# Kernel tuning notes

Hardware: AMD Instinct MI355X
Metric: run time of the kernel (lower is better)

Reference implementation:

```python
import jax, jax.numpy as jnp
import numpy as np

NUM_CLASSES = 1000
MARGIN = 1.0
COS_EPS = 1e-8   # torch F.cosine_similarity eps
NORM_EPS = 1e-12 # torch F.normalize eps


def setup_inputs() -> dict:
    key = jax.random.key(0)
    k1, k2 = jax.random.split(key)
    N, D = 65536, 256
    embeddings = jax.random.normal(k1, (N, D), dtype=jnp.float32)
    labels = jax.random.randint(k2, (N,), 0, NUM_CLASSES)
    return {"embeddings": embeddings, "labels": labels}


def reference(embeddings, labels):
    N = embeddings.shape[0]
    # L2-normalize embeddings (torch F.normalize with eps clamp on norm)
    e_norm = jnp.maximum(jnp.linalg.norm(embeddings, axis=1, keepdims=True), NORM_EPS)
    e = embeddings / e_norm  # [N, D], unit rows

    # Per-class mean of normalized embeddings; zero vector for empty classes
    sums = jax.ops.segment_sum(e, labels, num_segments=NUM_CLASSES)          # [C, D]
    counts = jax.ops.segment_sum(jnp.ones((N,), e.dtype), labels,
                                 num_segments=NUM_CLASSES)                    # [C]
    centers = sums / jnp.maximum(counts, 1.0)[:, None]                        # [C, D]

    # cosine_similarity(e_i, center_j) = (e_i . c_j) / max(||e_i||*||c_j||, eps)
    # ||e_i|| == 1 (up to the normalize clamp), so denom = max(||c_j||, eps)
    c_norm = jnp.linalg.norm(centers, axis=1)                                 # [C]
    denom = jnp.maximum(c_norm, COS_EPS)
    sims = (e @ centers.T) / denom[None, :]                                   # [N, C]

    rows = jnp.arange(N)
    pos = jnp.square(sims[rows, labels] - 1.0)                                # [N]
    neg_all = jnp.square(jax.nn.relu(MARGIN - sims))                          # [N, C]
    neg_at_label = neg_all[rows, labels]                                      # [N]
    neg = (neg_all.sum(axis=1) - neg_at_label) / (NUM_CLASSES - 1)            # [N]

    return jnp.mean(pos + neg)
```

## Files before the change

kernel.cpp:

```cpp
#include <hip/hip_runtime.h>
#include <hip/hip_bf16.h>

#define NROWS 65536
#define DIM   256
#define NCLS  1000
#define CPAD  1024

typedef __attribute__((ext_vector_type(8))) short bf16x8;
typedef __attribute__((ext_vector_type(4))) float f32x4;

__device__ inline unsigned short f2bf(float x) {
    unsigned int u = __builtin_bit_cast(unsigned int, x);
    unsigned int lsb = (u >> 16) & 1u;
    u += 0x7fffu + lsb;
    return (unsigned short)(u >> 16);
}

__device__ inline float bf2f(unsigned short u) {
    unsigned int v = ((unsigned int)u) << 16;
    return __builtin_bit_cast(float, v);
}

__device__ inline void gload_lds16(const void* g, void* l) {
    __builtin_amdgcn_global_load_lds(
        (const __attribute__((address_space(1))) unsigned int*)g,
        (__attribute__((address_space(3))) unsigned int*)l, 16, 0, 0);
}

__global__ __launch_bounds__(256) void k_norm_acc(
    const float* __restrict__ emb, const int* __restrict__ labels,
    unsigned short* __restrict__ e, unsigned int* __restrict__ counts)
{
    int gid  = blockIdx.x * 256 + threadIdx.x;
    int row  = gid >> 6;
    int lane = gid & 63;
    float4 v = ((const float4*)(emb + (size_t)row * DIM))[lane];
    float ss = v.x*v.x + v.y*v.y + v.z*v.z + v.w*v.w;
    #pragma unroll
    for (int off = 1; off < 64; off <<= 1) ss += __shfl_xor(ss, off);
    float inv = 1.0f / fmaxf(sqrtf(ss), 1e-12f);
    v.x *= inv; v.y *= inv; v.z *= inv; v.w *= inv;
    ushort4 u;
    u.x = f2bf(v.x); u.y = f2bf(v.y); u.z = f2bf(v.z); u.w = f2bf(v.w);
    ((ushort4*)(e + (size_t)row * DIM))[lane] = u;
    if (lane == 0) atomicAdd(counts + labels[row], 1u);
}

__global__ __launch_bounds__(1024) void k_prefix(
    const unsigned int* __restrict__ counts, unsigned int* __restrict__ offs,
    unsigned int* __restrict__ cursor)
{
    __shared__ unsigned int s[1024];
    int t = threadIdx.x;
    s[t] = (t < NCLS) ? counts[t] : 0u;
    __syncthreads();
    for (int d = 1; d < 1024; d <<= 1) {
        unsigned int v = (t >= d) ? s[t - d] : 0u;
        __syncthreads();
        s[t] += v;
        __syncthreads();
    }
    if (t < NCLS) {
        unsigned int excl = (t == 0) ? 0u : s[t - 1];
        offs[t]   = excl;
        cursor[t] = excl;
    }
}

__global__ __launch_bounds__(256) void k_scatter(
    const int* __restrict__ labels, unsigned int* __restrict__ cursor,
    int* __restrict__ sidx)
{
    int r = blockIdx.x * 256 + threadIdx.x;
    unsigned int pos = atomicAdd(&cursor[labels[r]], 1u);
    sidx[pos] = r;
}

__global__ __launch_bounds__(256) void k_gather_sum(
    const unsigned short* __restrict__ e, const int* __restrict__ sidx,
    const unsigned int* __restrict__ offs, const unsigned int* __restrict__ counts,
    float* __restrict__ sums)
{
    __shared__ int   sidx_s[256];
    __shared__ float part[4][256];
    const int tid  = threadIdx.x;
    const int wave = tid >> 6, lane = tid & 63;
    const int c    = blockIdx.x;
    unsigned int beg = offs[c], cnt = counts[c];

    float a0 = 0.f, a1 = 0.f, a2 = 0.f, a3 = 0.f;
    for (unsigned int base = 0; base < cnt; base += 256) {
        int m = (int)(cnt - base > 256u ? 256u : cnt - base);
        __syncthreads();
        if (tid < m) sidx_s[tid] = sidx[beg + base + tid];
        __syncthreads();
        for (int u = wave; u < m; u += 4) {
            ushort4 v = ((const ushort4*)(e + (size_t)sidx_s[u] * DIM))[lane];
            a0 += bf2f(v.x); a1 += bf2f(v.y); a2 += bf2f(v.z); a3 += bf2f(v.w);
        }
    }
    ((float4*)part[wave])[lane] = make_float4(a0, a1, a2, a3);
    __syncthreads();
    sums[(size_t)c * DIM + tid] =
        part[0][tid] + part[1][tid] + part[2][tid] + part[3][tid];
}

__global__ __launch_bounds__(256) void k_centers(
    const float* __restrict__ sums, const unsigned int* __restrict__ counts,
    unsigned short* __restrict__ cs)
{
    int gid  = blockIdx.x * 256 + threadIdx.x;
    int c    = gid >> 6;
    int lane = gid & 63;
    float4 v = make_float4(0.f, 0.f, 0.f, 0.f);
    if (c < NCLS) {
        v = ((const float4*)(sums + (size_t)c * DIM))[lane];
        float ic = 1.0f / fmaxf((float)counts[c], 1.0f);
        v.x *= ic; v.y *= ic; v.z *= ic; v.w *= ic;
        float ss = v.x*v.x + v.y*v.y + v.z*v.z + v.w*v.w;
        #pragma unroll
        for (int off = 1; off < 64; off <<= 1) ss += __shfl_xor(ss, off);
        float sc = 1.0f / fmaxf(sqrtf(ss), 1e-8f);
        v.x *= sc; v.y *= sc; v.z *= sc; v.w *= sc;
    }
    ushort4 u;
    u.x = f2bf(v.x); u.y = f2bf(v.y); u.z = f2bf(v.z); u.w = f2bf(v.w);
    ((ushort4*)(cs + (size_t)c * DIM))[lane] = u;
}

#define TMB 128
#define TCB 128

__global__ __launch_bounds__(256, 2) void k_loss_mfma(
    const unsigned short* __restrict__ e, const unsigned short* __restrict__ cs,
    const int* __restrict__ labels, float* __restrict__ acc)
{
    __shared__ __align__(16) unsigned short a_s[3][TMB * 64];
    __shared__ __align__(16) unsigned short b_s[2][TCB * 64];

    const int tid  = threadIdx.x;
    const int row0 = blockIdx.x * TMB;
    const int wave = tid >> 6, lane = tid & 63;
    const int wm = wave >> 1, wn = wave & 1;
    const int l16 = lane & 15, q = lane >> 4;
    const int st_r = lane >> 3;
    const int st_s = (lane & 7) ^ st_r;

    int labv[16];
    #pragma unroll
    for (int mi = 0; mi < 4; ++mi)
        #pragma unroll
        for (int rg = 0; rg < 4; ++rg)
            labv[mi * 4 + rg] = labels[row0 + wm*64 + mi*16 + q*4 + rg];

    #pragma unroll
    for (int kc = 0; kc < 3; ++kc)
        #pragma unroll
        for (int ch = 0; ch < 4; ++ch) {
            int chunk = wave * 4 + ch;
            int row   = chunk * 8 + st_r;
            gload_lds16(&e[(size_t)(row0 + row) * DIM + kc * 64 + st_s * 8],
                        &a_s[kc][chunk * 512]);
        }
    bf16x8 af3[4][2];
    #pragma unroll
    for (int mi = 0; mi < 4; ++mi) {
        const unsigned short* pa =
            e + (size_t)(row0 + wm*64 + mi*16 + l16) * DIM + 192 + q * 8;
        af3[mi][0] = *(const bf16x8*)pa;
        af3[mi][1] = *(const bf16x8*)(pa + 32);
    }
    #pragma unroll
    for (int ch = 0; ch < 4; ++ch) {
        int chunk = wave * 4 + ch;
        int row   = chunk * 8 + st_r;
        gload_lds16(&cs[(size_t)row * DIM + st_s * 8], &b_s[0][chunk * 512]);
    }
    __syncthreads();

    float la_bulk = 0.0f, la_corr = 0.0f;
    const float KN = 1.0f / 999.0f;
    f32x4 accf[4][4];

    for (int s = 0; s < 32; ++s) {
        const int cb = s >> 2, kc = s & 3;
        if (s < 31) {
            int s2 = s + 1;
            int cb2 = s2 >> 2, kc2 = s2 & 3;
            #pragma unroll
            for (int ch = 0; ch < 4; ++ch) {
                int chunk = wave * 4 + ch;
                int row   = chunk * 8 + st_r;
                gload_lds16(&cs[(size_t)(cb2 * TCB + row) * DIM + kc2 * 64 + st_s * 8],
                            &b_s[s2 & 1][chunk * 512]);
            }
        }
        if (kc == 0) {
            #pragma unroll
            for (int mi = 0; mi < 4; ++mi)
                #pragma unroll
                for (int ni = 0; ni < 4; ++ni)
                    accf[mi][ni] = (f32x4){0.f, 0.f, 0.f, 0.f};
        }
        const unsigned short* bs = b_s[s & 1];
        #pragma unroll
        for (int kk = 0; kk < 2; ++kk) {
            bf16x8 af[4], bfr[4];
            #pragma unroll
            for (int mi = 0; mi < 4; ++mi) {
                if (kc < 3) {
                    int rowA = wm*64 + mi*16 + l16;
                    af[mi] = *(const bf16x8*)&a_s[kc][
                        rowA*64 + (((kk*4 + q) ^ (rowA & 7)) * 8)];
                } else {
                    af[mi] = af3[mi][kk];
                }
            }
            #pragma unroll
            for (int ni = 0; ni < 4; ++ni) {
                int rowB = wn*64 + ni*16 + l16;
                bfr[ni] = *(const bf16x8*)&bs[rowB*64 + (((kk*4 + q) ^ (rowB & 7)) * 8)];
            }
            #pragma unroll
            for (int mi = 0; mi < 4; ++mi)
                #pragma unroll
                for (int ni = 0; ni < 4; ++ni)
                    accf[mi][ni] = __builtin_amdgcn_mfma_f32_16x16x32_bf16(
                        af[mi], bfr[ni], accf[mi][ni], 0, 0, 0);
        }
        if (kc == 3) {
            #pragma unroll
            for (int mi = 0; mi < 4; ++mi)
                #pragma unroll
                for (int rg = 0; rg < 4; ++rg) {
                    #pragma unroll
                    for (int ni = 0; ni < 4; ++ni) {
                        float t = 1.0f - accf[mi][ni][rg];
                        la_bulk += t * t;
                    }
                    int lr = labv[mi*4 + rg] - cb*128 - wn*64 - l16;
                    if ((lr & ~48) == 0) {
                        int nih = lr >> 4;
                        float sv = (nih == 0) ? accf[mi][0][rg] :
                                   (nih == 1) ? accf[mi][1][rg] :
                                   (nih == 2) ? accf[mi][2][rg] : accf[mi][3][rg];
                        float t = 1.0f - sv;
                        la_corr += t * t;
                    }
                }
        }
        __syncthreads();
    }

    float la = la_bulk * KN + la_corr * (1.0f - KN);
    #pragma unroll
    for (int off = 32; off >= 1; off >>= 1) la += __shfl_xor(la, off);
    float* red = (float*)&b_s[0][0];
    if (lane == 0) red[wave] = la;
    __syncthreads();
    if (tid == 0) atomicAdd(acc, red[0] + red[1] + red[2] + red[3]);
}

__global__ void k_final(const float* __restrict__ acc, float* __restrict__ out)
{
    if (threadIdx.x == 0)
        out[0] = acc[0] * (1.0f / (float)NROWS) - 24.0f * (1.0f / 999.0f);
}

extern "C" void kernel_launch(void* const* d_in, const int* in_sizes, int n_in,
                              void* d_out, int out_size, void* d_ws, size_t ws_size,
                              hipStream_t stream)
{
    const float* emb    = (const float*)d_in[0];
    const int*   labels = (const int*)d_in[1];
    float*       out    = (float*)d_out;
    char*        ws     = (char*)d_ws;

    const size_t OFF_SUMS = (size_t)NROWS * DIM * 2;
    const size_t OFF_CNT  = OFF_SUMS + (size_t)NCLS * DIM * 4;
    const size_t OFF_ACC  = OFF_CNT + 4096;
    const size_t OFF_OFFS = OFF_ACC + 16;
    const size_t OFF_CUR  = OFF_OFFS + 4096;
    const size_t OFF_SIDX = OFF_CUR + 4096;
    const size_t OFF_CS   = OFF_SIDX + (size_t)NROWS * 4;

    unsigned short* e      = (unsigned short*)ws;
    float*          sums   = (float*)(ws + OFF_SUMS);
    unsigned int*   counts = (unsigned int*)(ws + OFF_CNT);
    float*          acc    = (float*)(ws + OFF_ACC);
    unsigned int*   offs   = (unsigned int*)(ws + OFF_OFFS);
    unsigned int*   cursor = (unsigned int*)(ws + OFF_CUR);
    int*            sidx   = (int*)(ws + OFF_SIDX);
    unsigned short* cs     = (unsigned short*)(ws + OFF_CS);

    hipMemsetAsync(ws + OFF_CNT, 0, 4096 + 16, stream);

    k_norm_acc  <<<NROWS / 4, 256, 0, stream>>>(emb, labels, e, counts);
    k_prefix    <<<1, 1024, 0, stream>>>(counts, offs, cursor);
    k_scatter   <<<NROWS / 256, 256, 0, stream>>>(labels, cursor, sidx);
    k_gather_sum<<<NCLS, 256, 0, stream>>>(e, sidx, offs, counts, sums);
    k_centers   <<<CPAD / 4, 256, 0, stream>>>(sums, counts, cs);
    k_loss_mfma <<<NROWS / TMB, 256, 0, stream>>>(e, cs, labels, acc);
    k_final     <<<1, 64, 0, stream>>>(acc, out);
}
```

Measured before the change: 189.3 us.

## Fuse class-center pipeline into ballot-scan kernel and drop memset and final launches

Replaces the count/prefix/scatter/gather/centers chain with one kernel per class. Each block scans all labels with wave ballots and sums the matching normalized rows, then normalizes the center in place. The memset is replaced by zeroing acc/done inside the normalize kernel. The final kernel is replaced by a last-block-done atomic pattern in the loss kernel. The loss kernel also holds two of the four K-chunks of A in registers instead of one, which cuts its LDS footprint. The aim is to remove four kernel launches and their serialization. In exchange every class block rereads the full 256 KB label array (about 256 MB of total L2 traffic), and the larger register tile may add pressure.

Measured after the change: 203.6 us. 7.5% more time.

```diff
diff --git a/kernel.cpp b/kernel.cpp
--- a/kernel.cpp
+++ b/kernel.cpp
@@ -28,10 +28,11 @@
 }
 
 __global__ __launch_bounds__(256) void k_norm_acc(
-    const float* __restrict__ emb, const int* __restrict__ labels,
-    unsigned short* __restrict__ e, unsigned int* __restrict__ counts)
+    const float* __restrict__ emb, unsigned short* __restrict__ e,
+    float* __restrict__ acc, unsigned int* __restrict__ done)
 {
     int gid  = blockIdx.x * 256 + threadIdx.x;
+    if (gid == 0) { *acc = 0.0f; *done = 0u; }
     int row  = gid >> 6;
     int lane = gid & 63;
     float4 v = ((const float4*)(emb + (size_t)row * DIM))[lane];
@@ -43,89 +44,61 @@
     ushort4 u;
     u.x = f2bf(v.x); u.y = f2bf(v.y); u.z = f2bf(v.z); u.w = f2bf(v.w);
     ((ushort4*)(e + (size_t)row * DIM))[lane] = u;
-    if (lane == 0) atomicAdd(counts + labels[row], 1u);
-}
-
-__global__ __launch_bounds__(1024) void k_prefix(
-    const unsigned int* __restrict__ counts, unsigned int* __restrict__ offs,
-    unsigned int* __restrict__ cursor)
-{
-    __shared__ unsigned int s[1024];
-    int t = threadIdx.x;
-    s[t] = (t < NCLS) ? counts[t] : 0u;
-    __syncthreads();
-    for (int d = 1; d < 1024; d <<= 1) {
-        unsigned int v = (t >= d) ? s[t - d] : 0u;
-        __syncthreads();
-        s[t] += v;
-        __syncthreads();
-    }
-    if (t < NCLS) {
-        unsigned int excl = (t == 0) ? 0u : s[t - 1];
-        offs[t]   = excl;
-        cursor[t] = excl;
-    }
-}
-
-__global__ __launch_bounds__(256) void k_scatter(
-    const int* __restrict__ labels, unsigned int* __restrict__ cursor,
-    int* __restrict__ sidx)
-{
-    int r = blockIdx.x * 256 + threadIdx.x;
-    unsigned int pos = atomicAdd(&cursor[labels[r]], 1u);
-    sidx[pos] = r;
-}
-
-__global__ __launch_bounds__(256) void k_gather_sum(
-    const unsigned short* __restrict__ e, const int* __restrict__ sidx,
-    const unsigned int* __restrict__ offs, const unsigned int* __restrict__ counts,
-    float* __restrict__ sums)
-{
-    __shared__ int   sidx_s[256];
-    __shared__ float part[4][256];
+}
+
+__global__ __launch_bounds__(256) void k_gather_centers(
+    const unsigned short* __restrict__ e, const int* __restrict__ labels,
+    unsigned short* __restrict__ cs)
+{
+    const int c    = blockIdx.x;
     const int tid  = threadIdx.x;
     const int wave = tid >> 6, lane = tid & 63;
-    const int c    = blockIdx.x;
-    unsigned int beg = offs[c], cnt = counts[c];
+
+    if (c >= NCLS) {
+        if (tid < 32) ((uint4*)(cs + (size_t)c * DIM))[tid] = make_uint4(0,0,0,0);
+        return;
+    }
+
+    __shared__ float part[4][DIM];
+    __shared__ unsigned int cnt_s[4];
+    __shared__ float nred[4];
 
     float a0 = 0.f, a1 = 0.f, a2 = 0.f, a3 = 0.f;
-    for (unsigned int base = 0; base < cnt; base += 256) {
-        int m = (int)(cnt - base > 256u ? 256u : cnt - base);
-        __syncthreads();
-        if (tid < m) sidx_s[tid] = sidx[beg + base + tid];
-        __syncthreads();
-        for (int u = wave; u < m; u += 4) {
-            ushort4 v = ((const ushort4*)(e + (size_t)sidx_s[u] * DIM))[lane];
-            a0 += bf2f(v.x); a1 += bf2f(v.y); a2 += bf2f(v.z); a3 += bf2f(v.w);
+    unsigned int cnt = 0;
+
+    for (int it = 0; it < NROWS / 256 / 8; ++it) {
+        int lb[8];
+        #pragma unroll
+        for (int u = 0; u < 8; ++u)
+            lb[u] = labels[(it * 8 + u) * 256 + wave * 64 + lane];
+        #pragma unroll
+        for (int u = 0; u < 8; ++u) {
+            unsigned long long m = __ballot(lb[u] == c);
+            cnt += (unsigned int)__popcll(m);
+            while (m) {
+                int b = __ffsll((long long)m) - 1;
+                m &= m - 1;
+                int r = (it * 8 + u) * 256 + wave * 64 + b;
+                ushort4 v = ((const ushort4*)(e + (size_t)r * DIM))[lane];
+                a0 += bf2f(v.x); a1 += bf2f(v.y); a2 += bf2f(v.z); a3 += bf2f(v.w);
+            }
         }
     }
     ((float4*)part[wave])[lane] = make_float4(a0, a1, a2, a3);
-    __syncthreads();
-    sums[(size_t)c * DIM + tid] =
-        part[0][tid] + part[1][tid] + part[2][tid] + part[3][tid];
-}
-
-__global__ __launch_bounds__(256) void k_centers(
-    const float* __restrict__ sums, const unsigned int* __restrict__ counts,
-    unsigned short* __restrict__ cs)
-{
-    int gid  = blockIdx.x * 256 + threadIdx.x;
-    int c    = gid >> 6;
-    int lane = gid & 63;
-    float4 v = make_float4(0.f, 0.f, 0.f, 0.f);
-    if (c < NCLS) {
-        v = ((const float4*)(sums + (size_t)c * DIM))[lane];
-        float ic = 1.0f / fmaxf((float)counts[c], 1.0f);
-        v.x *= ic; v.y *= ic; v.z *= ic; v.w *= ic;
-        float ss = v.x*v.x + v.y*v.y + v.z*v.z + v.w*v.w;
-        #pragma unroll
-        for (int off = 1; off < 64; off <<= 1) ss += __shfl_xor(ss, off);
-        float sc = 1.0f / fmaxf(sqrtf(ss), 1e-8f);
-        v.x *= sc; v.y *= sc; v.z *= sc; v.w *= sc;
-    }
-    ushort4 u;
-    u.x = f2bf(v.x); u.y = f2bf(v.y); u.z = f2bf(v.z); u.w = f2bf(v.w);
-    ((ushort4*)(cs + (size_t)c * DIM))[lane] = u;
+    if (lane == 0) cnt_s[wave] = cnt;
+    __syncthreads();
+
+    float s  = part[0][tid] + part[1][tid] + part[2][tid] + part[3][tid];
+    float fc = (float)(cnt_s[0] + cnt_s[1] + cnt_s[2] + cnt_s[3]);
+    float v  = s * (1.0f / fmaxf(fc, 1.0f));
+    float vv = v * v;
+    #pragma unroll
+    for (int off = 32; off >= 1; off >>= 1) vv += __shfl_xor(vv, off);
+    if (lane == 0) nred[wave] = vv;
+    __syncthreads();
+    float ss = nred[0] + nred[1] + nred[2] + nred[3];
+    float sc = 1.0f / fmaxf(sqrtf(ss), 1e-8f);
+    cs[(size_t)c * DIM + tid] = f2bf(v * sc);
 }
 
 #define TMB 128
@@ -133,10 +106,12 @@
 
 __global__ __launch_bounds__(256, 2) void k_loss_mfma(
     const unsigned short* __restrict__ e, const unsigned short* __restrict__ cs,
-    const int* __restrict__ labels, float* __restrict__ acc)
-{
-    __shared__ __align__(16) unsigned short a_s[3][TMB * 64];
+    const int* __restrict__ labels, float* __restrict__ acc,
+    unsigned int* __restrict__ done, float* __restrict__ out)
+{
+    __shared__ __align__(16) unsigned short a_s[2][TMB * 64];
     __shared__ __align__(16) unsigned short b_s[2][TCB * 64];
+    __shared__ float red_s[4];
 
     const int tid  = threadIdx.x;
     const int row0 = blockIdx.x * TMB;
@@ -154,7 +129,7 @@
             labv[mi * 4 + rg] = labels[row0 + wm*64 + mi*16 + q*4 + rg];
 
     #pragma unroll
-    for (int kc = 0; kc < 3; ++kc)
+    for (int kc = 0; kc < 2; ++kc)
         #pragma unroll
         for (int ch = 0; ch < 4; ++ch) {
             int chunk = wave * 4 + ch;
@@ -162,13 +137,16 @@
             gload_lds16(&e[(size_t)(row0 + row) * DIM + kc * 64 + st_s * 8],
                         &a_s[kc][chunk * 512]);
         }
-    bf16x8 af3[4][2];
+    bf16x8 af23[2][4][2];
     #pragma unroll
     for (int mi = 0; mi < 4; ++mi) {
         const unsigned short* pa =
-            e + (size_t)(row0 + wm*64 + mi*16 + l16) * DIM + 192 + q * 8;
-        af3[mi][0] = *(const bf16x8*)pa;
-        af3[mi][1] = *(const bf16x8*)(pa + 32);
+            e + (size_t)(row0 + wm*64 + mi*16 + l16) * DIM + 128 + q * 8;
+        #pragma unroll
+        for (int kh = 0; kh < 2; ++kh) {
+            af23[kh][mi][0] = *(const bf16x8*)(pa + kh * 64);
+            af23[kh][mi][1] = *(const bf16x8*)(pa + kh * 64 + 32);
+        }
     }
     #pragma unroll
     for (int ch = 0; ch < 4; ++ch) {
@@ -208,12 +186,12 @@
             bf16x8 af[4], bfr[4];
             #pragma unroll
             for (int mi = 0; mi < 4; ++mi) {
-                if (kc < 3) {
+                if (kc < 2) {
                     int rowA = wm*64 + mi*16 + l16;
                     af[mi] = *(const bf16x8*)&a_s[kc][
                         rowA*64 + (((kk*4 + q) ^ (rowA & 7)) * 8)];
                 } else {
-                    af[mi] = af3[mi][kk];
+                    af[mi] = af23[kc - 2][mi][kk];
                 }
             }
             #pragma unroll
@@ -255,16 +233,17 @@
     float la = la_bulk * KN + la_corr * (1.0f - KN);
     #pragma unroll
     for (int off = 32; off >= 1; off >>= 1) la += __shfl_xor(la, off);
-    float* red = (float*)&b_s[0][0];
-    if (lane == 0) red[wave] = la;
-    __syncthreads();
-    if (tid == 0) atomicAdd(acc, red[0] + red[1] + red[2] + red[3]);
-}
-
-__global__ void k_final(const float* __restrict__ acc, float* __restrict__ out)
-{
-    if (threadIdx.x == 0)
-        out[0] = acc[0] * (1.0f / (float)NROWS) - 24.0f * (1.0f / 999.0f);
+    if (lane == 0) red_s[wave] = la;
+    __syncthreads();
+    if (tid == 0) {
+        atomicAdd(acc, red_s[0] + red_s[1] + red_s[2] + red_s[3]);
+        __threadfence();
+        unsigned int t = atomicAdd(done, 1u);
+        if (t == (unsigned int)(NROWS / TMB) - 1u) {
+            float v = atomicAdd(acc, 0.0f);
+            out[0] = v * (1.0f / (float)NROWS) - 24.0f * (1.0f / 999.0f);
+        }
+    }
 }
 
 extern "C" void kernel_launch(void* const* d_in, const int* in_sizes, int n_in,
@@ -276,30 +255,16 @@
     float*       out    = (float*)d_out;
     char*        ws     = (char*)d_ws;
 
-    const size_t OFF_SUMS = (size_t)NROWS * DIM * 2;
-    const size_t OFF_CNT  = OFF_SUMS + (size_t)NCLS * DIM * 4;
-    const size_t OFF_ACC  = OFF_CNT + 4096;
-    const size_t OFF_OFFS = OFF_ACC + 16;
-    const size_t OFF_CUR  = OFF_OFFS + 4096;
-    const size_t OFF_SIDX = OFF_CUR + 4096;
-    const size_t OFF_CS   = OFF_SIDX + (size_t)NROWS * 4;
-
-    unsigned short* e      = (unsigned short*)ws;
-    float*          sums   = (float*)(ws + OFF_SUMS);
-    unsigned int*   counts = (unsigned int*)(ws + OFF_CNT);
-    float*          acc    = (float*)(ws + OFF_ACC);
-    unsigned int*   offs   = (unsigned int*)(ws + OFF_OFFS);
-    unsigned int*   cursor = (unsigned int*)(ws + OFF_CUR);
-    int*            sidx   = (int*)(ws + OFF_SIDX);
-    unsigned short* cs     = (unsigned short*)(ws + OFF_CS);
-
-    hipMemsetAsync(ws + OFF_CNT, 0, 4096 + 16, stream);
-
-    k_norm_acc  <<<NROWS / 4, 256, 0, stream>>>(emb, labels, e, counts);
-    k_prefix    <<<1, 1024, 0, stream>>>(counts, offs, cursor);
-    k_scatter   <<<NROWS / 256, 256, 0, stream>>>(labels, cursor, sidx);
-    k_gather_sum<<<NCLS, 256, 0, stream>>>(e, sidx, offs, counts, sums);
-    k_centers   <<<CPAD / 4, 256, 0, stream>>>(sums, counts, cs);
-    k_loss_mfma <<<NROWS / TMB, 256, 0, stream>>>(e, cs, labels, acc);
-    k_final     <<<1, 64, 0, stream>>>(acc, out);
-}
+    const size_t OFF_CS   = (size_t)NROWS * DIM * 2;
+    const size_t OFF_ACC  = OFF_CS + (size_t)CPAD * DIM * 2;
+    const size_t OFF_DONE = OFF_ACC + 16;
+
+    unsigned short* e    = (unsigned short*)ws;
+    unsigned short* cs   = (unsigned short*)(ws + OFF_CS);
+    float*          acc  = (float*)(ws + OFF_ACC);
+    unsigned int*   done = (unsigned int*)(ws + OFF_DONE);
+
+    k_norm_acc      <<<NROWS / 4, 256, 0, stream>>>(emb, e, acc, done);
+    k_gather_centers<<<CPAD, 256, 0, stream>>>(e, labels, cs);
+    k_loss_mfma     <<<NROWS / TMB, 256, 0, stream>>>(e, cs, labels, acc, done, out);
+}
```
